# Kernel tuning notes

Hardware: AMD Instinct MI355X
Metric: run time of the kernel (lower is better)

The kernel has to match this reference:

```python
import jax, jax.numpy as jnp
import numpy as np


def setup_inputs() -> dict:
    key = jax.random.key(0)
    ks = jax.random.split(key, 7)
    t, e, h = 2048, 512, 8
    s = 0.02
    return {
        "x": jax.random.normal(ks[0], (t, e), jnp.float32),
        "y": jax.random.normal(ks[1], (t, e), jnp.float32),
        "Wk": jax.random.normal(ks[2], (e, e * h), jnp.float32) * s,
        "Wq": jax.random.normal(ks[3], (e, e * h), jnp.float32) * s,
        "Wv": jax.random.normal(ks[4], (e, e * h), jnp.float32) * s,
        "Wu": jax.random.normal(ks[5], (e * h, e), jnp.float32) * s,
        "bu": jnp.zeros((e,), jnp.float32),
    }


def reference(x, y, Wk, Wq, Wv, Wu, bu):
    t, e = x.shape
    h = Wk.shape[1] // e
    scale = e ** (-0.25)
    # projections -> [h, t, e] (head dim equals emb in this 'wide' attention)
    k = (x @ Wk).reshape(t, h, e).transpose(1, 0, 2) * scale
    q = (y @ Wq).reshape(t, h, e).transpose(1, 0, 2) * scale
    v = (x @ Wv).reshape(t, h, e).transpose(1, 0, 2)
    # scores [h, t, t]
    dot = jnp.einsum('hte,hse->hts', q, k)
    attn = jax.nn.softmax(dot, axis=-1)
    out = jnp.einsum('hts,hse->hte', attn, v)          # [h, t, e]
    out = out.transpose(1, 0, 2).reshape(t, h * e)     # [t, h*e]
    return (out @ Wu + bu)[None]                       # [1, t, e] (b=1 in original)
```

## Files before the change

### kernel.cpp

```cpp
#include <hip/hip_runtime.h>
#include <hip/hip_bf16.h>
#include <stdint.h>

#define T_SEQ 2048
#define EMB   512
#define NH    8
#define HEAD_ALL 4096

typedef __attribute__((ext_vector_type(8))) short short8;
typedef __attribute__((ext_vector_type(4))) float f32x4;

__device__ __forceinline__ unsigned short f2b(float f) {
    __hip_bfloat16 h = __float2bfloat16(f);
    return *reinterpret_cast<unsigned short*>(&h);
}
__device__ __forceinline__ float b2f(unsigned short u) {
    return __uint_as_float(((unsigned)u) << 16);
}
__device__ __forceinline__ void gload_lds16(const void* g, void* l) {
    __builtin_amdgcn_global_load_lds((__attribute__((address_space(1))) void*)(void*)(g),
                                     (__attribute__((address_space(3))) void*)(l), 16, 0, 0);
}
__device__ __forceinline__ void wg_barrier() {
    asm volatile("" ::: "memory");
    __builtin_amdgcn_s_barrier();
    asm volatile("" ::: "memory");
}

__global__ void cvt_bf16_2(const float* __restrict__ a, const float* __restrict__ b,
                           unsigned short* __restrict__ oa, unsigned short* __restrict__ ob, int n8) {
    const float* in = blockIdx.y ? b : a;
    unsigned short* out = blockIdx.y ? ob : oa;
    int i = blockIdx.x * 256 + threadIdx.x;
    if (i >= n8) return;
    const f32x4* p = (const f32x4*)in + 2 * (size_t)i;
    f32x4 va = p[0], vb = p[1];
    uint4 o;
    o.x = (unsigned)f2b(va[0]) | ((unsigned)f2b(va[1]) << 16);
    o.y = (unsigned)f2b(va[2]) | ((unsigned)f2b(va[3]) << 16);
    o.z = (unsigned)f2b(vb[0]) | ((unsigned)f2b(vb[1]) << 16);
    o.w = (unsigned)f2b(vb[2]) | ((unsigned)f2b(vb[3]) << 16);
    *((uint4*)out + i) = o;
}

__global__ void transpose_cvt3_f32(const float* __restrict__ w0, const float* __restrict__ w1,
                                   const float* __restrict__ w2, unsigned short* __restrict__ out,
                                   int R, int C, long outS) {
    __shared__ unsigned short t[64][66];
    const int z = blockIdx.z;
    const float* in = (z == 0) ? w0 : ((z == 1) ? w1 : w2);
    unsigned short* ob = out + (long)z * outS;
    const int tid = threadIdx.x;
    const int r0 = blockIdx.y * 64, c0 = blockIdx.x * 64;
#pragma unroll
    for (int it = 0; it < 4; ++it) {
        int flat = it * 256 + tid;
        int r = flat >> 4, c4 = flat & 15;
        f32x4 v = *(const f32x4*)(in + (long)(r0 + r) * C + c0 + c4 * 4);
#pragma unroll
        for (int w = 0; w < 4; ++w) t[r][c4 * 4 + w] = f2b(v[w]);
    }
    __syncthreads();
#pragma unroll
    for (int it = 0; it < 2; ++it) {
        int flat = it * 256 + tid;
        int rr = flat >> 3, c8 = flat & 7;
        unsigned u[4];
#pragma unroll
        for (int w = 0; w < 4; ++w) {
            unsigned short a = t[c8 * 8 + 2 * w][rr];
            unsigned short b = t[c8 * 8 + 2 * w + 1][rr];
            u[w] = (unsigned)a | ((unsigned)b << 16);
        }
        *(uint4*)(ob + (long)(c0 + rr) * R + r0 + c8 * 8) = make_uint4(u[0], u[1], u[2], u[3]);
    }
}

__global__ void transpose_bf16(const unsigned short* __restrict__ in, unsigned short* __restrict__ out,
                               int R, int C, long inS, long outS) {
    __shared__ unsigned short t[64][66];
    const unsigned short* ib = in + (long)blockIdx.z * inS;
    unsigned short* ob = out + (long)blockIdx.z * outS;
    const int tid = threadIdx.x;
    const int r0 = blockIdx.y * 64, c0 = blockIdx.x * 64;
#pragma unroll
    for (int it = 0; it < 2; ++it) {
        int flat = it * 256 + tid;
        int r = flat >> 3, c8 = flat & 7;
        uint4 v = *(const uint4*)(ib + (long)(r0 + r) * C + c0 + c8 * 8);
        unsigned u[4] = {v.x, v.y, v.z, v.w};
#pragma unroll
        for (int w = 0; w < 4; ++w) {
            t[r][c8 * 8 + 2 * w]     = (unsigned short)(u[w] & 0xffff);
            t[r][c8 * 8 + 2 * w + 1] = (unsigned short)(u[w] >> 16);
        }
    }
    __syncthreads();
#pragma unroll
    for (int it = 0; it < 2; ++it) {
        int flat = it * 256 + tid;
        int rr = flat >> 3, c8 = flat & 7;
        unsigned u[4];
#pragma unroll
        for (int w = 0; w < 4; ++w)
            u[w] = (unsigned)t[c8 * 8 + 2 * w][rr] | ((unsigned)t[c8 * 8 + 2 * w + 1][rr] << 16);
        *(uint4*)(ob + (long)(c0 + rr) * R + r0 + c8 * 8) = make_uint4(u[0], u[1], u[2], u[3]);
    }
}

template<int R_>
__device__ __forceinline__ void stage2(const unsigned short* __restrict__ src, int kfull,
                                       short* ldsbase, int i, int tid, int wid) {
#pragma unroll
    for (int s = 0; s < 2; ++s) {
        const int ii = i + s;
        const int r = ii * 64 + (tid >> 3);
        const int d = (tid & 7) * 16;
        const int sc = (d ^ ((r & 7) << 4)) >> 1;
        gload_lds16(src + (long)r * kfull + sc, ldsbase + ii * 4096 + wid * 512);
    }
}

template<int BM, int BN, int KTILES, int MODE>
__global__ __launch_bounds__(512, 2)
void gemm8p(const unsigned short* __restrict__ A, const unsigned short* __restrict__ A2,
            const unsigned short* __restrict__ B, void* __restrict__ Cout,
            int kfull, float alpha, long As, long Bs, long Cs, int ldc)
{
    static_assert(KTILES >= 3, "pipeline needs >=3 K-tiles");
    constexpr int ATILE = BM * 64;
    constexpr int BTILE = BN * 64;
    constexpr int LA = BM / 64;
    constexpr int LB = BN / 64;
    constexpr int MF = BM / 32;
    constexpr int NF = BN / 64;
    constexpr int MFP = MF / 4;

    __shared__ __align__(16) short lds[2 * (ATILE + BTILE)];

    const int tid = threadIdx.x;
    const int wid = tid >> 6, lane = tid & 63;
    const int wm = wid >> 2, wn = wid & 3;
    const int fr = lane & 15, fq = lane >> 4;

    const int nwg = gridDim.x * gridDim.y * gridDim.z;
    int flat = blockIdx.x + gridDim.x * (blockIdx.y + gridDim.y * blockIdx.z);
    flat = (flat & 7) * (nwg >> 3) + (flat >> 3);
    const int bx = flat % gridDim.x;
    const int rem = flat / gridDim.x;
    const int by = rem % gridDim.y;
    const long batch = rem / gridDim.y;

    const int bm = by * BM, bn = bx * BN;

    const unsigned short* Ab;
    const unsigned short* Bb;
    int koff = 0;
    if constexpr (MODE == 1) { Ab = (batch == 2) ? A2 : A; Bb = B + batch * Bs; }
    else { Ab = A; Bb = B; koff = (int)batch * (KTILES * 64); }

    const unsigned short* Ag = Ab + (long)bm * kfull + koff;
    const unsigned short* Bg = Bb + (long)bn * kfull + koff;

    f32x4 acc[MF][NF];
#pragma unroll
    for (int i = 0; i < MF; i++)
#pragma unroll
        for (int j = 0; j < NF; j++) acc[i][j] = 0.f;

#pragma unroll
    for (int i = 0; i < LA; i += 2) stage2<BM>(Ag, kfull, lds, i, tid, wid);
#pragma unroll
    for (int i = 0; i < LB; i += 2) stage2<BN>(Bg, kfull, lds + 2 * ATILE, i, tid, wid);
#pragma unroll
    for (int i = 0; i < LB; i += 2) stage2<BN>(Bg + 64, kfull, lds + 2 * ATILE + BTILE, i, tid, wid);
    if constexpr (LB == 4) asm volatile("s_waitcnt vmcnt(4)" ::: "memory");
    else                   asm volatile("s_waitcnt vmcnt(2)" ::: "memory");
    wg_barrier();

#pragma unroll 2
    for (int t = 0; t < KTILES; ++t) {
        short* la  = lds + (t & 1) * ATILE;
        short* laN = lds + ((t + 1) & 1) * ATILE;
        short* lb  = lds + 2 * ATILE + (t & 1) * BTILE;
        const int kA = (t + 1) * 64;
        const int kB = (t + 2) * 64;

        short8 bfrag[NF][2];
#pragma unroll
        for (int q = 0; q < 4; ++q) {
            if (q == 0) {
#pragma unroll
                for (int nf = 0; nf < NF; ++nf)
#pragma unroll
                    for (int kk = 0; kk < 2; ++kk) {
                        const int r = wn * (BN / 4) + nf * 16 + fr;
                        const int cb = kk * 64 + fq * 16;
                        bfrag[nf][kk] = *(const short8*)(lb + r * 64 + ((cb ^ ((r & 7) << 4)) >> 1));
                    }
            }
            short8 afrag[MFP][2];
#pragma unroll
            for (int mf = 0; mf < MFP; ++mf)
#pragma unroll
                for (int kk = 0; kk < 2; ++kk) {
                    const int r = wm * (BM / 2) + q * (BM / 8) + mf * 16 + fr;
                    const int cb = kk * 64 + fq * 16;
                    afrag[mf][kk] = *(const short8*)(la + r * 64 + ((cb ^ ((r & 7) << 4)) >> 1));
                }
            if (t + 1 < KTILES) {
                if (q == 0) stage2<BM>(Ag + kA, kfull, laN, 0, tid, wid);
                if (q == 1 && LA == 4) stage2<BM>(Ag + kA, kfull, laN, 2, tid, wid);
            }
            if (t + 2 < KTILES) {
                if (q == 2) stage2<BN>(Bg + kB, kfull, lb, 0, tid, wid);
                if (q == 3 && LB == 4) stage2<BN>(Bg + kB, kfull, lb, 2, tid, wid);
            }
            wg_barrier();
            __builtin_amdgcn_s_setprio(1);
#pragma unroll
            for (int mf = 0; mf < MFP; ++mf)
#pragma unroll
                for (int nf = 0; nf < NF; ++nf)
#pragma unroll
                    for (int kk = 0; kk < 2; ++kk)
                        acc[q * MFP + mf][nf] = __builtin_amdgcn_mfma_f32_16x16x32_bf16(
                            afrag[mf][kk], bfrag[nf][kk], acc[q * MFP + mf][nf], 0, 0, 0);
            __builtin_amdgcn_s_setprio(0);
            if (q == 3) {
                if (t + 2 < KTILES) {
                    if constexpr (LB == 4) asm volatile("s_waitcnt vmcnt(4)" ::: "memory");
                    else                   asm volatile("s_waitcnt vmcnt(2)" ::: "memory");
                } else {
                    asm volatile("s_waitcnt vmcnt(0)" ::: "memory");
                }
            }
            wg_barrier();
        }
    }

#pragma unroll
    for (int m = 0; m < MF; ++m)
#pragma unroll
        for (int j = 0; j < 4; ++j) {
            const int row = bm + wm * (BM / 2) + m * 16 + fq * 4 + j;
#pragma unroll
            for (int n = 0; n < NF; ++n) {
                const int col = bn + wn * (BN / 4) + n * 16 + fr;
                const float v = acc[m][n][j] * alpha;
                if constexpr (MODE == 1) {
                    unsigned short* C = (unsigned short*)Cout + batch * Cs;
                    C[(long)(col >> 9) * ((long)T_SEQ * EMB) + (long)row * EMB + (col & 511)] = f2b(v);
                } else {
                    float* C = (float*)Cout + batch * ((long)T_SEQ * EMB);
                    C[(long)row * ldc + col] = v;
                }
            }
        }
}

__global__ __launch_bounds__(512, 2)
void attn_fused(const unsigned short* __restrict__ Qg, const unsigned short* __restrict__ Kg,
                const unsigned short* __restrict__ VTg, unsigned short* __restrict__ Og,
                float scale)
{
    __shared__ __align__(16) short lds[69888];
    float* rs = (float*)(lds + 69632);
    char* ldsb = (char*)lds;

    const int tid = threadIdx.x;
    const int wid = tid >> 6, lane = tid & 63;
    const int fr = lane & 15, fq = lane >> 4;
    const int rg = wid >> 1, ch = wid & 1;

    const int orig = blockIdx.x + 32 * blockIdx.y;
    const int f = (orig & 7) * 32 + (orig >> 3);
    const int qb = f & 31, h = f >> 5;
    const long TE = (long)T_SEQ * EMB;
    const unsigned short* Qh = Qg + (long)h * TE + (long)(qb * 64) * EMB;
    const unsigned short* Kh = Kg + (long)h * TE;
    const unsigned short* Vh = VTg + (long)h * TE;

    short8 qreg[16];
#pragma unroll
    for (int ks = 0; ks < 16; ++ks)
        qreg[ks] = *(const short8*)(Qh + (long)(rg * 16 + fr) * EMB + ks * 32 + fq * 8);

    auto stageK = [&](int kb) {
#pragma unroll
        for (int it = 0; it < 8; ++it) {
            const int c = it * 512 + tid;
            const int kv = c >> 6, s = c & 63;
            gload_lds16(Kh + (long)(kb * 64 + kv) * EMB + (((s * 16) ^ ((kv & 7) << 4)) >> 1),
                        lds + (it * 512 + wid * 64) * 8);
        }
    };
    auto stageV = [&](int kb) {
#pragma unroll
        for (int it = 0; it < 8; ++it) {
            const int c = it * 512 + tid;
            const int d = c >> 3, s = c & 7;
            gload_lds16(Vh + (long)d * T_SEQ + kb * 64 + (((s * 16) ^ ((d & 7) << 4)) >> 1),
                        lds + 32768 + (it * 512 + wid * 64) * 8);
        }
    };

    f32x4 oacc[4][4];
#pragma unroll
    for (int m = 0; m < 4; ++m)
#pragma unroll
        for (int n = 0; n < 4; ++n) oacc[m][n] = 0.f;
    float rsum[4] = {0.f, 0.f, 0.f, 0.f};

    stageK(0);
    stageV(0);

#pragma unroll 1
    for (int t = 0; t < 32; ++t) {
        asm volatile("s_waitcnt vmcnt(8)" ::: "memory");
        wg_barrier();

        f32x4 sacc[2][2];
#pragma unroll
        for (int c = 0; c < 2; ++c) { sacc[c][0] = 0.f; sacc[c][1] = 0.f; }
#pragma unroll
        for (int ks = 0; ks < 16; ++ks) {
#pragma unroll
            for (int c = 0; c < 2; ++c) {
                const int kv = (ch * 2 + c) * 16 + fr;
                const short8 bfr = *(const short8*)(ldsb + kv * 1024 +
                                    (((ks * 64 + fq * 16)) ^ ((kv & 7) << 4)));
                sacc[c][ks & 1] = __builtin_amdgcn_mfma_f32_16x16x32_bf16(
                    qreg[ks], bfr, sacc[c][ks & 1], 0, 0, 0);
            }
        }
#pragma unroll
        for (int c = 0; c < 2; ++c)
#pragma unroll
            for (int j = 0; j < 4; ++j) {
                const float v = __expf(scale * (sacc[c][0][j] + sacc[c][1][j]));
                rsum[j] += v;
                const int row = rg * 16 + fq * 4 + j;
                const int kv = (ch * 2 + c) * 16 + fr;
                *(unsigned short*)(ldsb + 131072 + row * 128 + ((kv * 2) ^ ((row & 7) << 4))) = f2b(v);
            }
        asm volatile("s_waitcnt lgkmcnt(0)" ::: "memory");
        asm volatile("s_waitcnt vmcnt(0)" ::: "memory");
        wg_barrier();
        if (t + 1 < 32) stageK(t + 1);

#pragma unroll
        for (int kk = 0; kk < 2; ++kk) {
            short8 sa[4], vb[4];
#pragma unroll
            for (int m = 0; m < 4; ++m) {
                const int row = m * 16 + fr;
                sa[m] = *(const short8*)(ldsb + 131072 + row * 128 +
                          ((kk * 64 + fq * 16) ^ ((row & 7) << 4)));
            }
#pragma unroll
            for (int n = 0; n < 4; ++n) {
                const int d = wid * 64 + n * 16 + fr;
                vb[n] = *(const short8*)(ldsb + 65536 + d * 128 +
                          ((kk * 64 + fq * 16) ^ ((d & 7) << 4)));
            }
            __builtin_amdgcn_s_setprio(1);
#pragma unroll
            for (int m = 0; m < 4; ++m)
#pragma unroll
                for (int n = 0; n < 4; ++n)
                    oacc[m][n] = __builtin_amdgcn_mfma_f32_16x16x32_bf16(
                        sa[m], vb[n], oacc[m][n], 0, 0, 0);
            __builtin_amdgcn_s_setprio(0);
        }
        wg_barrier();
        if (t + 1 < 32) stageV(t + 1);
    }

#pragma unroll
    for (int j = 0; j < 4; ++j) {
        float v = rsum[j];
        v += __shfl_xor(v, 1);
        v += __shfl_xor(v, 2);
        v += __shfl_xor(v, 4);
        v += __shfl_xor(v, 8);
        if (fr == 0) rs[ch * 64 + rg * 16 + fq * 4 + j] = v;
    }
    asm volatile("s_waitcnt lgkmcnt(0)" ::: "memory");
    wg_barrier();

#pragma unroll
    for (int m = 0; m < 4; ++m)
#pragma unroll
        for (int j = 0; j < 4; ++j) {
            const int row = m * 16 + fq * 4 + j;
            const float rinv = 1.0f / (rs[row] + rs[64 + row]);
#pragma unroll
            for (int n = 0; n < 4; ++n) {
                const int d = wid * 64 + n * 16 + fr;
                Og[(long)(qb * 64 + row) * HEAD_ALL + h * EMB + d] = f2b(oacc[m][n][j] * rinv);
            }
        }
}

__global__ void reduce_bias(const float* __restrict__ part, const float* __restrict__ bias,
                            float* __restrict__ out) {
    const int i = blockIdx.x * 256 + threadIdx.x;
    const long stride4 = (long)T_SEQ * EMB / 4;
    const f32x4* p = (const f32x4*)part;
    f32x4 s = p[i];
#pragma unroll
    for (int sl = 1; sl < 8; ++sl) s += p[i + sl * stride4];
    f32x4 b = *(const f32x4*)(bias + ((i * 4) % EMB));
    *((f32x4*)out + i) = s + b;
}

extern "C" void kernel_launch(void* const* d_in, const int* in_sizes, int n_in,
                              void* d_out, int out_size, void* d_ws, size_t ws_size,
                              hipStream_t stream)
{
    const float* x  = (const float*)d_in[0];
    const float* y  = (const float*)d_in[1];
    const float* Wk = (const float*)d_in[2];
    const float* Wq = (const float*)d_in[3];
    const float* Wv = (const float*)d_in[4];
    const float* Wu = (const float*)d_in[5];
    const float* bu = (const float*)d_in[6];
    char* ws = (char*)d_ws;
    const size_t MB = 1024ull * 1024ull;

    unsigned short* xb   = (unsigned short*)(ws + 0);
    unsigned short* yb   = (unsigned short*)(ws + 2 * MB);
    unsigned short* WT3  = (unsigned short*)(ws + 4 * MB);
    unsigned short* PRJ  = (unsigned short*)(ws + 48 * MB);
    unsigned short* Vb   = (unsigned short*)(ws + 48 * MB);
    unsigned short* Kb   = (unsigned short*)(ws + 64 * MB);
    unsigned short* Qb   = (unsigned short*)(ws + 80 * MB);
    unsigned short* WuT  = (unsigned short*)(ws + 96 * MB);
    unsigned short* VTb  = (unsigned short*)(ws + 100 * MB);
    unsigned short* Ob   = (unsigned short*)(ws + 116 * MB);
    float*          part = (float*)(ws + 0);

    const float scale2 = 0.04419417382415922f;
    const long TE = (long)T_SEQ * EMB;

    cvt_bf16_2<<<dim3(512, 2), dim3(256), 0, stream>>>(x, y, xb, yb, T_SEQ * EMB / 8);
    transpose_cvt3_f32<<<dim3(HEAD_ALL / 64, EMB / 64, 3), dim3(256), 0, stream>>>(
        Wv, Wk, Wq, WT3, EMB, HEAD_ALL, (long)2 * MB);
    transpose_cvt3_f32<<<dim3(EMB / 64, HEAD_ALL / 64, 1), dim3(256), 0, stream>>>(
        Wu, nullptr, nullptr, WuT, HEAD_ALL, EMB, 0);

    gemm8p<256, 256, 8, 1><<<dim3(HEAD_ALL / 256, T_SEQ / 256, 3), 512, 0, stream>>>(
        xb, yb, WT3, PRJ, EMB, 1.f, 0, (long)2 * MB, (long)8 * MB, 0);

    transpose_bf16<<<dim3(EMB / 64, T_SEQ / 64, NH), dim3(256), 0, stream>>>(
        Vb, VTb, T_SEQ, EMB, TE, TE);

    attn_fused<<<dim3(32, 8), 512, 0, stream>>>(Qb, Kb, VTb, Ob, scale2);

    gemm8p<256, 128, 8, 3><<<dim3(EMB / 128, T_SEQ / 256, 8), 512, 0, stream>>>(
        Ob, nullptr, WuT, part, HEAD_ALL, 1.f, 0, 0, 0, EMB);

    reduce_bias<<<dim3(T_SEQ * EMB / 4 / 256), dim3(256), 0, stream>>>(part, bu, (float*)d_out);
}
```

Baseline: 181.2 us.

## Remap QK^T warp tiling so each warp reuses K fragment across two Q rows

Changes the QK^T warp partition from 4 row-groups × 2 column halves to 2 row-groups × 4 column chunks, so each warp holds two 16-row Q fragments in registers and reuses one K LDS fragment for two MFMAs. This halves K-tile LDS reads in the score stage but doubles Q register footprint (32 short8). The P-tile LDS swizzle gains an extra XOR bit to avoid bank conflicts, and the row-sum reduction now combines four partial sums per row.

```diff
diff --git a/kernel.cpp b/kernel.cpp
--- a/kernel.cpp
+++ b/kernel.cpp
@@ -264,14 +264,14 @@
                 const unsigned short* __restrict__ VTg, unsigned short* __restrict__ Og,
                 float scale)
 {
-    __shared__ __align__(16) short lds[69888];
+    __shared__ __align__(16) short lds[70144];
     float* rs = (float*)(lds + 69632);
     char* ldsb = (char*)lds;
 
     const int tid = threadIdx.x;
     const int wid = tid >> 6, lane = tid & 63;
     const int fr = lane & 15, fq = lane >> 4;
-    const int rg = wid >> 1, ch = wid & 1;
+    const int rg = wid & 1, ch = wid >> 1;
 
     const int orig = blockIdx.x + 32 * blockIdx.y;
     const int f = (orig & 7) * 32 + (orig >> 3);
@@ -281,10 +281,12 @@
     const unsigned short* Kh = Kg + (long)h * TE;
     const unsigned short* Vh = VTg + (long)h * TE;
 
-    short8 qreg[16];
-#pragma unroll
-    for (int ks = 0; ks < 16; ++ks)
-        qreg[ks] = *(const short8*)(Qh + (long)(rg * 16 + fr) * EMB + ks * 32 + fq * 8);
+    short8 qreg[2][16];
+#pragma unroll
+    for (int mm = 0; mm < 2; ++mm)
+#pragma unroll
+        for (int ks = 0; ks < 16; ++ks)
+            qreg[mm][ks] = *(const short8*)(Qh + (long)(rg * 32 + mm * 16 + fr) * EMB + ks * 32 + fq * 8);
 
     auto stageK = [&](int kb) {
 #pragma unroll
@@ -310,7 +312,11 @@
     for (int m = 0; m < 4; ++m)
 #pragma unroll
         for (int n = 0; n < 4; ++n) oacc[m][n] = 0.f;
-    float rsum[4] = {0.f, 0.f, 0.f, 0.f};
+    float rsum[2][4];
+#pragma unroll
+    for (int mm = 0; mm < 2; ++mm)
+#pragma unroll
+        for (int j = 0; j < 4; ++j) rsum[mm][j] = 0.f;
 
     stageK(0);
     stageV(0);
@@ -322,27 +328,26 @@
 
         f32x4 sacc[2][2];
 #pragma unroll
-        for (int c = 0; c < 2; ++c) { sacc[c][0] = 0.f; sacc[c][1] = 0.f; }
+        for (int mm = 0; mm < 2; ++mm) { sacc[mm][0] = 0.f; sacc[mm][1] = 0.f; }
+        const int kv = ch * 16 + fr;
 #pragma unroll
         for (int ks = 0; ks < 16; ++ks) {
-#pragma unroll
-            for (int c = 0; c < 2; ++c) {
-                const int kv = (ch * 2 + c) * 16 + fr;
-                const short8 bfr = *(const short8*)(ldsb + kv * 1024 +
-                                    (((ks * 64 + fq * 16)) ^ ((kv & 7) << 4)));
-                sacc[c][ks & 1] = __builtin_amdgcn_mfma_f32_16x16x32_bf16(
-                    qreg[ks], bfr, sacc[c][ks & 1], 0, 0, 0);
-            }
-        }
-#pragma unroll
-        for (int c = 0; c < 2; ++c)
+            const short8 bfr = *(const short8*)(ldsb + kv * 1024 +
+                                ((ks * 64 + fq * 16) ^ ((kv & 7) << 4)));
+#pragma unroll
+            for (int mm = 0; mm < 2; ++mm)
+                sacc[mm][ks & 1] = __builtin_amdgcn_mfma_f32_16x16x32_bf16(
+                    qreg[mm][ks], bfr, sacc[mm][ks & 1], 0, 0, 0);
+        }
+#pragma unroll
+        for (int mm = 0; mm < 2; ++mm)
 #pragma unroll
             for (int j = 0; j < 4; ++j) {
-                const float v = __expf(scale * (sacc[c][0][j] + sacc[c][1][j]));
-                rsum[j] += v;
-                const int row = rg * 16 + fq * 4 + j;
-                const int kv = (ch * 2 + c) * 16 + fr;
-                *(unsigned short*)(ldsb + 131072 + row * 128 + ((kv * 2) ^ ((row & 7) << 4))) = f2b(v);
+                const float v = __expf(scale * (sacc[mm][0][j] + sacc[mm][1][j]));
+                rsum[mm][j] += v;
+                const int row = rg * 32 + mm * 16 + fq * 4 + j;
+                *(unsigned short*)(ldsb + 131072 + row * 128 +
+                    ((kv * 2) ^ ((row & 7) << 4) ^ ((row & 8) << 2))) = f2b(v);
             }
         asm volatile("s_waitcnt lgkmcnt(0)" ::: "memory");
         asm volatile("s_waitcnt vmcnt(0)" ::: "memory");
@@ -356,7 +361,7 @@
             for (int m = 0; m < 4; ++m) {
                 const int row = m * 16 + fr;
                 sa[m] = *(const short8*)(ldsb + 131072 + row * 128 +
-                          ((kk * 64 + fq * 16) ^ ((row & 7) << 4)));
+                          ((kk * 64 + fq * 16) ^ ((row & 7) << 4) ^ ((row & 8) << 2)));
             }
 #pragma unroll
             for (int n = 0; n < 4; ++n) {
@@ -378,14 +383,16 @@
     }
 
 #pragma unroll
-    for (int j = 0; j < 4; ++j) {
-        float v = rsum[j];
-        v += __shfl_xor(v, 1);
-        v += __shfl_xor(v, 2);
-        v += __shfl_xor(v, 4);
-        v += __shfl_xor(v, 8);
-        if (fr == 0) rs[ch * 64 + rg * 16 + fq * 4 + j] = v;
-    }
+    for (int mm = 0; mm < 2; ++mm)
+#pragma unroll
+        for (int j = 0; j < 4; ++j) {
+            float v = rsum[mm][j];
+            v += __shfl_xor(v, 1);
+            v += __shfl_xor(v, 2);
+            v += __shfl_xor(v, 4);
+            v += __shfl_xor(v, 8);
+            if (fr == 0) rs[ch * 64 + rg * 32 + mm * 16 + fq * 4 + j] = v;
+        }
     asm volatile("s_waitcnt lgkmcnt(0)" ::: "memory");
     wg_barrier();
 
@@ -394,7 +401,7 @@
 #pragma unroll
         for (int j = 0; j < 4; ++j) {
             const int row = m * 16 + fq * 4 + j;
-            const float rinv = 1.0f / (rs[row] + rs[64 + row]);
+            const float rinv = 1.0f / (rs[row] + rs[64 + row] + rs[128 + row] + rs[192 + row]);
 #pragma unroll
             for (int n = 0; n < 4; ++n) {
                 const int d = wid * 64 + n * 16 + fr;
```

Result: slower. 277.8 us (+53.3%).
